# Performance work log

Hardware: AMD Instinct MI355X
Metric: run time of the kernel (lower is better)

## Reference

```python
import jax, jax.numpy as jnp
import numpy as np

EPS = 1e-8

def _l2norm(x):
    # normalize rows, guarding against zero norm like torch cosine similarity eps
    n = jnp.sqrt(jnp.sum(x * x, axis=-1, keepdims=True))
    return x / jnp.maximum(n, EPS)

def setup_inputs() -> dict:
    key = jax.random.key(0)
    k1, k2, k3 = jax.random.split(key, 3)
    Nq, Nk, D = 4096, 4096, 1024
    return {
        "queries": jax.random.normal(k1, (Nq, D), dtype=jnp.float32),
        "keys": jax.random.normal(k2, (Nk, D), dtype=jnp.float32),
        "values": jax.random.normal(k3, (Nk, D), dtype=jnp.float32),
    }

def reference(queries, keys, values):
    # CosineSimilarityMatrix(keys, queries): [Nk, Nq] pairwise cosine sims
    attn_weights = jnp.matmul(_l2norm(keys), _l2norm(queries).T)  # [Nk, Nq]
    # weighted sum over keys for each query
    weighted = jnp.matmul(attn_weights.T, values)  # [Nq, D]
    return (weighted, attn_weights)
```

## Files before the change

kernel.cpp:

```cpp
#include <hip/hip_runtime.h>


typedef unsigned short u16;
typedef unsigned int u32;
typedef unsigned char u8;
typedef float f32x4 __attribute__((ext_vector_type(4)));
typedef int int4v __attribute__((ext_vector_type(4)));
typedef __bf16 bf16x8 __attribute__((ext_vector_type(8)));

__device__ __forceinline__ u16 f2bf(float f) {
  u32 u = __builtin_bit_cast(u32, f);
  return (u16)((u + 0x7FFFu + ((u >> 16) & 1u)) >> 16);
}

__device__ __forceinline__ void gload16(const u16* g, u16* l) {
  __builtin_amdgcn_global_load_lds((__attribute__((address_space(1))) void*)(void*)g,
                                   (__attribute__((address_space(3))) void*)(void*)l, 16, 0, 0);
}
__device__ __forceinline__ void gload16b(const u8* g, u8* l) {
  __builtin_amdgcn_global_load_lds((__attribute__((address_space(1))) void*)(void*)g,
                                   (__attribute__((address_space(3))) void*)(void*)l, 16, 0, 0);
}

#define BARRIER() __builtin_amdgcn_s_barrier()
#define WAITVM(n) asm volatile("s_waitcnt vmcnt(" #n ")" ::: "memory")
#define WAITLGKM0() do { asm volatile("s_waitcnt lgkmcnt(0)" ::: "memory"); \
                         __builtin_amdgcn_sched_barrier(0); } while (0)

__global__ __launch_bounds__(256) void norm_transv_kernel(
    const float* __restrict__ q, const float* __restrict__ k,
    u16* __restrict__ qnb, u16* __restrict__ knb,
    u8* __restrict__ qnq, u8* __restrict__ knq,
    float* __restrict__ sclQ, float* __restrict__ sclK,
    const float* __restrict__ v, u16* __restrict__ vbT) {
  int bid = blockIdx.x, t = threadIdx.x;
  if (bid < 8192) {
    const bool isQ = (bid < 4096);
    const float* src = isQ ? q : k;
    u16* dst = isQ ? qnb : knb;
    u8* dst8 = isQ ? qnq : knq;
    float* scl = isQ ? sclQ : sclK;
    int row = bid & 4095;
    const float4 val = ((const float4*)(src + (size_t)row * 1024))[t];
    float s = val.x * val.x + val.y * val.y + val.z * val.z + val.w * val.w;
    float am = fmaxf(fmaxf(fabsf(val.x), fabsf(val.y)), fmaxf(fabsf(val.z), fabsf(val.w)));
    #pragma unroll
    for (int off = 32; off > 0; off >>= 1) {
      s += __shfl_xor(s, off, 64);
      am = fmaxf(am, __shfl_xor(am, off, 64));
    }
    __shared__ float2 red[4];
    if ((t & 63) == 0) red[t >> 6] = make_float2(s, am);
    __syncthreads();
    float tot = red[0].x + red[1].x + red[2].x + red[3].x;
    float amall = fmaxf(fmaxf(red[0].y, red[1].y), fmaxf(red[2].y, red[3].y));
    float inv = 1.0f / fmaxf(sqrtf(tot), 1e-8f);
    float rm = fmaxf(amall * inv, 1e-30f);
    float iq = 127.0f / rm;
    uint2 o;
    o.x = (u32)f2bf(val.x * inv) | ((u32)f2bf(val.y * inv) << 16);
    o.y = (u32)f2bf(val.z * inv) | ((u32)f2bf(val.w * inv) << 16);
    *(uint2*)(dst + (size_t)row * 1024 + t * 4) = o;
    int c0 = (int)rintf(val.x * inv * iq);
    int c1 = (int)rintf(val.y * inv * iq);
    int c2 = (int)rintf(val.z * inv * iq);
    int c3 = (int)rintf(val.w * inv * iq);
    u32 p = (u32)(c0 & 255) | ((u32)(c1 & 255) << 8) |
            ((u32)(c2 & 255) << 16) | ((u32)(c3 & 255) << 24);
    ((u32*)(dst8 + (size_t)row * 1024))[t] = p;
    if (t == 0) scl[row] = rm * (1.0f / 127.0f);
  } else {
    __shared__ __align__(16) float lds[64 * 64];
    int tix = bid - 8192;
    int r0 = (tix >> 4) * 64, c0 = (tix & 15) * 64;
    int ch = t & 15, lr = t >> 4;
    #pragma unroll
    for (int i = 0; i < 4; ++i) {
      int r = lr + i * 16;
      float4 val = *(const float4*)&v[(size_t)(r0 + r) * 1024 + c0 + ch * 4];
      int byteoff = r * 256 + ((ch * 16) ^ (((r >> 3) & 7) << 4));
      *(float4*)((char*)lds + byteoff) = val;
    }
    __syncthreads();
    int cch = t & 7, lrow = t >> 3;
    #pragma unroll
    for (int i = 0; i < 2; ++i) {
      int oc = lrow + i * 32;
      u16 vals[8];
      #pragma unroll
      for (int j = 0; j < 8; ++j) {
        int srl = cch * 8 + j;
        int byteoff = srl * 256 + (((oc >> 2) * 16) ^ (((srl >> 3) & 7) << 4)) + (oc & 3) * 4;
        vals[j] = f2bf(*(const float*)((const char*)lds + byteoff));
      }
      uint4 o;
      o.x = (u32)vals[0] | ((u32)vals[1] << 16);
      o.y = (u32)vals[2] | ((u32)vals[3] << 16);
      o.z = (u32)vals[4] | ((u32)vals[5] << 16);
      o.w = (u32)vals[6] | ((u32)vals[7] << 16);
      *(uint4*)&vbT[(size_t)(c0 + oc) * 4096 + r0 + cch * 8] = o;
    }
  }
}

__global__ __launch_bounds__(256) void transpose_bf16_kernel(
    const u16* __restrict__ src, u16* __restrict__ dst) {
  int b = blockIdx.x;
  int r0 = (b >> 4) * 64, c0 = (b & 15) * 64;
  __shared__ __align__(16) u16 lds[64 * 64];
  int t = threadIdx.x;
  int lrow = t >> 3, cch = t & 7;
  #pragma unroll
  for (int i = 0; i < 2; ++i) {
    int sr = lrow + i * 32;
    uint4 val = *(const uint4*)&src[(size_t)(r0 + sr) * 1024 + c0 + cch * 8];
    int byteoff = sr * 128 + ((cch * 16) ^ (((sr >> 3) & 7) << 4));
    *(uint4*)((char*)lds + byteoff) = val;
  }
  __syncthreads();
  #pragma unroll
  for (int i = 0; i < 2; ++i) {
    int oc = lrow + i * 32;
    u16 vals[8];
    #pragma unroll
    for (int j = 0; j < 8; ++j) {
      int srl = cch * 8 + j;
      int byteoff = srl * 128 + ((oc * 2) ^ (cch << 4));
      vals[j] = *(const u16*)((const char*)lds + byteoff);
    }
    uint4 o;
    o.x = (u32)vals[0] | ((u32)vals[1] << 16);
    o.y = (u32)vals[2] | ((u32)vals[3] << 16);
    o.z = (u32)vals[4] | ((u32)vals[5] << 16);
    o.w = (u32)vals[6] | ((u32)vals[7] << 16);
    *(uint4*)&dst[(size_t)(c0 + oc) * 4096 + r0 + cch * 8] = o;
  }
}

template<int BM, int BN, int MW, int NW>
__global__ __launch_bounds__(256) void gemm_abt(
    const u16* __restrict__ A, const u16* __restrict__ B, float* __restrict__ Cptr,
    int k_len, int lda, int ldb, int ldc, int plane) {
  static_assert(BM == 2 * MW * 16 && BN == 2 * NW * 16, "wave grid is 2x2");
  static_assert(BM / 32 + BN / 32 == 6, "WAITVM(6) literal assumes 6 loads/thread/stage");
  constexpr int TILE = (BM + BN) * 64;
  __shared__ __align__(16) u16 lds[3 * TILE];
  const int t = threadIdx.x, l = t & 63, w = t >> 6;
  const int tileM = blockIdx.y, tileN = blockIdx.x;
  const int k_start = blockIdx.z * k_len;
  Cptr += (size_t)blockIdx.z * plane;
  const int srow = l >> 3;
  const int cswz = ((l & 7) ^ srow) * 8;
  const u16* gA = A + (size_t)(tileM * BM) * lda + k_start + cswz;
  const u16* gB = B + (size_t)(tileN * BN) * ldb + k_start + cswz;
  const int slot0 = (l >> 4) ^ (l & 7);
  const int aoff0 = ((w >> 1) * MW * 16 + (l & 15)) * 64 + slot0 * 8;
  const int aoff1 = ((w >> 1) * MW * 16 + (l & 15)) * 64 + (slot0 ^ 4) * 8;
  const int boff0 = BM * 64 + ((w & 1) * NW * 16 + (l & 15)) * 64 + slot0 * 8;
  const int boff1 = BM * 64 + ((w & 1) * NW * 16 + (l & 15)) * 64 + (slot0 ^ 4) * 8;

  f32x4 acc[MW][NW];
  #pragma unroll
  for (int m = 0; m < MW; ++m)
    #pragma unroll
    for (int n = 0; n < NW; ++n) acc[m][n] = (f32x4){0.f, 0.f, 0.f, 0.f};

  auto stage = [&](int buf, int kof) {
    u16* bb = lds + buf * TILE;
    #pragma unroll
    for (int j = 0; j < BM / 32; ++j) {
      const int r = w * (BM / 4) + j * 8;
      gload16(gA + (size_t)(r + srow) * lda + kof, bb + r * 64);
    }
    #pragma unroll
    for (int j = 0; j < BN / 32; ++j) {
      const int r = w * (BN / 4) + j * 8;
      gload16(gB + (size_t)(r + srow) * ldb + kof, bb + BM * 64 + r * 64);
    }
  };

  bf16x8 av0[MW], bv0[NW], av1[MW], bv1[NW];
  const int nt = k_len >> 6;
  stage(0, 0);
  if (nt > 1) { stage(1, 64); WAITVM(6); }
  else        { WAITVM(0); }
  BARRIER();
  #pragma unroll
  for (int m = 0; m < MW; ++m) av0[m] = *(const bf16x8*)&lds[aoff0 + m * 1024];
  #pragma unroll
  for (int n = 0; n < NW; ++n) bv0[n] = *(const bf16x8*)&lds[boff0 + n * 1024];

  for (int i = 0; i < nt; ++i) {
    const u16* bb = lds + (i % 3) * TILE;
    if (i + 2 < nt) stage((i + 2) % 3, (i + 2) * 64);
    #pragma unroll
    for (int m = 0; m < MW; ++m) av1[m] = *(const bf16x8*)&bb[aoff1 + m * 1024];
    #pragma unroll
    for (int n = 0; n < NW; ++n) bv1[n] = *(const bf16x8*)&bb[boff1 + n * 1024];
    #pragma unroll
    for (int m = 0; m < MW; ++m)
      #pragma unroll
      for (int n = 0; n < NW; ++n)
        acc[m][n] = __builtin_amdgcn_mfma_f32_16x16x32_bf16(av0[m], bv0[n], acc[m][n], 0, 0, 0);
    #pragma unroll
    for (int m = 0; m < MW; ++m)
      #pragma unroll
      for (int n = 0; n < NW; ++n)
        acc[m][n] = __builtin_amdgcn_mfma_f32_16x16x32_bf16(av1[m], bv1[n], acc[m][n], 0, 0, 0);
    if (i + 1 < nt) {
      if (i + 2 < nt) { WAITVM(6); } else { WAITVM(0); }
    }
    BARRIER();
    if (i + 1 < nt) {
      const u16* nb = lds + ((i + 1) % 3) * TILE;
      #pragma unroll
      for (int m = 0; m < MW; ++m) av0[m] = *(const bf16x8*)&nb[aoff0 + m * 1024];
      #pragma unroll
      for (int n = 0; n < NW; ++n) bv0[n] = *(const bf16x8*)&nb[boff0 + n * 1024];
    }
  }

  const int orow = tileM * BM + (w >> 1) * MW * 16 + (l >> 4) * 4;
  const int ocol = tileN * BN + (w & 1) * NW * 16 + (l & 15);
  #pragma unroll
  for (int m = 0; m < MW; ++m)
    #pragma unroll
    for (int n = 0; n < NW; ++n)
      #pragma unroll
      for (int r = 0; r < 4; ++r)
        Cptr[(size_t)(orow + m * 16 + r) * ldc + (ocol + n * 16)] = acc[m][n][r];
}

__global__ __launch_bounds__(512, 2) void gemm256_i8(
    const u8* __restrict__ A8, const u8* __restrict__ B8, float* __restrict__ C,
    const float* __restrict__ P, u16* __restrict__ ctred,
    const float* __restrict__ sclK, const float* __restrict__ sclQ, int ntn) {
  __shared__ __align__(16) u8 lds8[131072];
  const int tid = threadIdx.x, l = tid & 63, w = tid >> 6;
  const int wm = w >> 2, wn = w & 3;
  const int nwg = gridDim.x * gridDim.y;
  const int bid = blockIdx.y * gridDim.x + blockIdx.x;
  const int swz = (bid & 7) * (nwg >> 3) + (bid >> 3);
  const int tileM = swz / ntn, tileN = swz % ntn;

  const int srow8 = l >> 3;
  const int cswzB = ((l & 7) ^ srow8) * 16;
  const u8* gA8 = A8 + (size_t)tileM * 256 * 1024 + cswzB;
  const u8* gB8 = B8 + (size_t)tileN * 256 * 1024 + cswzB;

#define STGJ(j, koff, bb) do { \
    gload16b(gA8 + (size_t)(w * 8 + 64 * (j) + srow8) * 1024 + (koff), \
             lds8 + (bb) + w * 1024 + (j) * 8192); \
    gload16b(gB8 + (size_t)(w * 8 + 64 * (j) + srow8) * 1024 + (koff), \
             lds8 + (bb) + 32768 + w * 1024 + (j) * 8192); } while (0)

  STGJ(0, 0, 0); STGJ(1, 0, 0); STGJ(2, 0, 0); STGJ(3, 0, 0);
  {
    const int base = bid * 4096 + tid * 8;
    f32x4 sa = *(const f32x4*)&P[base];
    f32x4 sb = *(const f32x4*)&P[base + 4];
    #pragma unroll
    for (int p = 1; p < 4; ++p) {
      sa += *(const f32x4*)&P[(size_t)p * 1048576 + base];
      sb += *(const f32x4*)&P[(size_t)p * 1048576 + base + 4];
    }
    uint4 o;
    o.x = (u32)f2bf(sa[0]) | ((u32)f2bf(sa[1]) << 16);
    o.y = (u32)f2bf(sa[2]) | ((u32)f2bf(sa[3]) << 16);
    o.z = (u32)f2bf(sb[0]) | ((u32)f2bf(sb[1]) << 16);
    o.w = (u32)f2bf(sb[2]) | ((u32)f2bf(sb[3]) << 16);
    *(uint4*)&ctred[base] = o;
  }
  WAITVM(0);
  BARRIER();

  const int fs = ((l >> 4) ^ (l & 7)) * 16;
  const int afrag0 = (wm * 128 + (l & 15)) * 128 + fs;
  const int bfrag0 = 32768 + (wn * 64 + (l & 15)) * 128 + fs;

  int4v acc[8][4];
  #pragma unroll
  for (int m = 0; m < 8; ++m)
    #pragma unroll
    for (int n = 0; n < 4; ++n) acc[m][n] = (int4v){0, 0, 0, 0};

#define MFMA16(AF, BF, MB) do { \
    __builtin_amdgcn_s_setprio(1); \
    _Pragma("unroll") \
    for (int m = 0; m < 4; ++m) { \
      _Pragma("unroll") \
      for (int n = 0; n < 4; ++n) \
        acc[(MB) + m][n] = __builtin_amdgcn_mfma_i32_16x16x64_i8(AF[m], BF[n], acc[(MB) + m][n], 0, 0, 0); \
    } \
    __builtin_amdgcn_s_setprio(0); } while (0)

  int4v A0[4], A1[4], B0[4], B1[4];
  #pragma unroll
  for (int m = 0; m < 4; ++m) A0[m] = *(const int4v*)&lds8[afrag0 + m * 2048];
  #pragma unroll
  for (int n = 0; n < 4; ++n) B0[n] = *(const int4v*)&lds8[bfrag0 + n * 2048];

  const int NT = 8;
  for (int t = 0; t < NT; ++t) {
    const int bb = (t & 1) << 16, nb = bb ^ 65536;
    const int nkoff = (t + 1) * 128;
    if (t + 1 < NT) STGJ(0, nkoff, nb);
    #pragma unroll
    for (int m = 0; m < 4; ++m) A1[m] = *(const int4v*)&lds8[bb + (afrag0 + (m + 4) * 2048)];
    WAITLGKM0();
    MFMA16(A0, B0, 0);
    if (t + 1 < NT) STGJ(1, nkoff, nb);
    #pragma unroll
    for (int m = 0; m < 4; ++m) A0[m] = *(const int4v*)&lds8[bb + ((afrag0 ^ 64) + m * 2048)];
    #pragma unroll
    for (int n = 0; n < 4; ++n) B1[n] = *(const int4v*)&lds8[bb + ((bfrag0 ^ 64) + n * 2048)];
    WAITLGKM0();
    MFMA16(A1, B0, 4);
    if (t + 1 < NT) STGJ(2, nkoff, nb);
    #pragma unroll
    for (int m = 0; m < 4; ++m) A1[m] = *(const int4v*)&lds8[bb + ((afrag0 ^ 64) + (m + 4) * 2048)];
    WAITLGKM0();
    MFMA16(A0, B1, 0);
    if (t + 1 < NT) STGJ(3, nkoff, nb);
    MFMA16(A1, B1, 4);
    if (t + 1 < NT) {
      WAITVM(0);
      BARRIER();
      #pragma unroll
      for (int m = 0; m < 4; ++m) A0[m] = *(const int4v*)&lds8[nb + (afrag0 + m * 2048)];
      #pragma unroll
      for (int n = 0; n < 4; ++n) B0[n] = *(const int4v*)&lds8[nb + (bfrag0 + n * 2048)];
    }
  }

  const int orow = tileM * 256 + wm * 128 + (l >> 4) * 4;
  const int ocol = tileN * 256 + wn * 64 + (l & 15);
  float sq[4];
  #pragma unroll
  for (int n = 0; n < 4; ++n) sq[n] = sclQ[ocol + n * 16];
  #pragma unroll
  for (int m = 0; m < 8; ++m) {
    const float4 sk4 = *(const float4*)&sclK[orow + m * 16];
    #pragma unroll
    for (int n = 0; n < 4; ++n)
      #pragma unroll
      for (int r = 0; r < 4; ++r)
        C[(size_t)(orow + m * 16 + r) * 4096 + (ocol + n * 16)] =
            (float)acc[m][n][r] * ((const float*)&sk4)[r] * sq[n];
  }
#undef STGJ
#undef MFMA16
}

extern "C" void kernel_launch(void* const* d_in, const int* in_sizes, int n_in,
                              void* d_out, int out_size, void* d_ws, size_t ws_size,
                              hipStream_t stream) {
  const float* q = (const float*)d_in[0];
  const float* k = (const float*)d_in[1];
  const float* v = (const float*)d_in[2];
  float* out = (float*)d_out;
  float* weighted = out;
  float* attn = out + 4194304;

  char* ws = (char*)d_ws;
  u16* qnb = (u16*)(ws);
  u16* knb = (u16*)(ws + (8u << 20));
  u16* knT = (u16*)(ws + (16u << 20));
  u16* vbT = (u16*)(ws + (24u << 20));
  u16* ct  = (u16*)(ws + (32u << 20));
  u8*  qnq = (u8*)(ws + (34u << 20));
  u8*  knq = (u8*)(ws + (38u << 20));
  float* sclQ = (float*)(ws + (42u << 20));
  float* sclK = (float*)(ws + (42u << 20) + 65536);

  norm_transv_kernel<<<9216, 256, 0, stream>>>(q, k, qnb, knb, qnq, knq, sclQ, sclK, v, vbT);
  transpose_bf16_kernel<<<1024, 256, 0, stream>>>(knb, knT);
  gemm_abt<128, 64, 4, 2><<<dim3(16, 8, 4), 256, 0, stream>>>(
      vbT, knT, weighted, 1024, 4096, 4096, 1024, 1048576);
  gemm256_i8<<<dim3(16, 16), 512, 0, stream>>>(
      knq, qnq, attn, weighted, ct, sclK, sclQ, 16);
  gemm_abt<128, 64, 4, 2><<<dim3(16, 32, 1), 256, 0, stream>>>(
      qnb, ct, weighted, 1024, 1024, 1024, 1024, 0);
}
```

Baseline: 82.50 us.

## Build transposed normalized K directly from fp32 keys and drop explicit LDS waits

New measurement: 83.07 us (median of 3 runs). No clear change (+0.7%).

```diff
diff --git a/kernel.cpp b/kernel.cpp
--- a/kernel.cpp
+++ b/kernel.cpp
@@ -24,20 +24,17 @@
 
 #define BARRIER() __builtin_amdgcn_s_barrier()
 #define WAITVM(n) asm volatile("s_waitcnt vmcnt(" #n ")" ::: "memory")
-#define WAITLGKM0() do { asm volatile("s_waitcnt lgkmcnt(0)" ::: "memory"); \
-                         __builtin_amdgcn_sched_barrier(0); } while (0)
 
 __global__ __launch_bounds__(256) void norm_transv_kernel(
     const float* __restrict__ q, const float* __restrict__ k,
-    u16* __restrict__ qnb, u16* __restrict__ knb,
+    u16* __restrict__ qnb,
     u8* __restrict__ qnq, u8* __restrict__ knq,
-    float* __restrict__ sclQ, float* __restrict__ sclK,
+    float* __restrict__ sclQ, float* __restrict__ sclK, float* __restrict__ invK,
     const float* __restrict__ v, u16* __restrict__ vbT) {
   int bid = blockIdx.x, t = threadIdx.x;
   if (bid < 8192) {
     const bool isQ = (bid < 4096);
     const float* src = isQ ? q : k;
-    u16* dst = isQ ? qnb : knb;
     u8* dst8 = isQ ? qnq : knq;
     float* scl = isQ ? sclQ : sclK;
     int row = bid & 4095;
@@ -57,10 +54,12 @@
     float inv = 1.0f / fmaxf(sqrtf(tot), 1e-8f);
     float rm = fmaxf(amall * inv, 1e-30f);
     float iq = 127.0f / rm;
-    uint2 o;
-    o.x = (u32)f2bf(val.x * inv) | ((u32)f2bf(val.y * inv) << 16);
-    o.y = (u32)f2bf(val.z * inv) | ((u32)f2bf(val.w * inv) << 16);
-    *(uint2*)(dst + (size_t)row * 1024 + t * 4) = o;
+    if (isQ) {
+      uint2 o;
+      o.x = (u32)f2bf(val.x * inv) | ((u32)f2bf(val.y * inv) << 16);
+      o.y = (u32)f2bf(val.z * inv) | ((u32)f2bf(val.w * inv) << 16);
+      *(uint2*)(qnb + (size_t)row * 1024 + t * 4) = o;
+    }
     int c0 = (int)rintf(val.x * inv * iq);
     int c1 = (int)rintf(val.y * inv * iq);
     int c2 = (int)rintf(val.z * inv * iq);
@@ -68,7 +67,10 @@
     u32 p = (u32)(c0 & 255) | ((u32)(c1 & 255) << 8) |
             ((u32)(c2 & 255) << 16) | ((u32)(c3 & 255) << 24);
     ((u32*)(dst8 + (size_t)row * 1024))[t] = p;
-    if (t == 0) scl[row] = rm * (1.0f / 127.0f);
+    if (t == 0) {
+      scl[row] = rm * (1.0f / 127.0f);
+      if (!isQ) invK[row] = inv;
+    }
   } else {
     __shared__ __align__(16) float lds[64 * 64];
     int tix = bid - 8192;
@@ -103,21 +105,26 @@
   }
 }
 
-__global__ __launch_bounds__(256) void transpose_bf16_kernel(
-    const u16* __restrict__ src, u16* __restrict__ dst) {
+__global__ __launch_bounds__(256) void transpose_k_kernel(
+    const float* __restrict__ k, const float* __restrict__ invK,
+    u16* __restrict__ knT) {
   int b = blockIdx.x;
   int r0 = (b >> 4) * 64, c0 = (b & 15) * 64;
-  __shared__ __align__(16) u16 lds[64 * 64];
+  __shared__ __align__(16) float lds[64 * 64];
   int t = threadIdx.x;
-  int lrow = t >> 3, cch = t & 7;
-  #pragma unroll
-  for (int i = 0; i < 2; ++i) {
-    int sr = lrow + i * 32;
-    uint4 val = *(const uint4*)&src[(size_t)(r0 + sr) * 1024 + c0 + cch * 8];
-    int byteoff = sr * 128 + ((cch * 16) ^ (((sr >> 3) & 7) << 4));
-    *(uint4*)((char*)lds + byteoff) = val;
+  int ch = t & 15, lr = t >> 4;
+  #pragma unroll
+  for (int i = 0; i < 4; ++i) {
+    int r = lr + i * 16;
+    float4 val = *(const float4*)&k[(size_t)(r0 + r) * 1024 + c0 + ch * 4];
+    int byteoff = r * 256 + ((ch * 16) ^ (((r >> 3) & 7) << 4));
+    *(float4*)((char*)lds + byteoff) = val;
   }
   __syncthreads();
+  int cch = t & 7, lrow = t >> 3;
+  float invv[8];
+  *(float4*)&invv[0] = *(const float4*)&invK[r0 + cch * 8];
+  *(float4*)&invv[4] = *(const float4*)&invK[r0 + cch * 8 + 4];
   #pragma unroll
   for (int i = 0; i < 2; ++i) {
     int oc = lrow + i * 32;
@@ -125,15 +132,15 @@
     #pragma unroll
     for (int j = 0; j < 8; ++j) {
       int srl = cch * 8 + j;
-      int byteoff = srl * 128 + ((oc * 2) ^ (cch << 4));
-      vals[j] = *(const u16*)((const char*)lds + byteoff);
+      int byteoff = srl * 256 + (((oc >> 2) * 16) ^ (((srl >> 3) & 7) << 4)) + (oc & 3) * 4;
+      vals[j] = f2bf(*(const float*)((const char*)lds + byteoff) * invv[j]);
     }
     uint4 o;
     o.x = (u32)vals[0] | ((u32)vals[1] << 16);
     o.y = (u32)vals[2] | ((u32)vals[3] << 16);
     o.z = (u32)vals[4] | ((u32)vals[5] << 16);
     o.w = (u32)vals[6] | ((u32)vals[7] << 16);
-    *(uint4*)&dst[(size_t)(c0 + oc) * 4096 + r0 + cch * 8] = o;
+    *(uint4*)&knT[(size_t)(c0 + oc) * 4096 + r0 + cch * 8] = o;
   }
 }
 
@@ -307,19 +314,16 @@
     if (t + 1 < NT) STGJ(0, nkoff, nb);
     #pragma unroll
     for (int m = 0; m < 4; ++m) A1[m] = *(const int4v*)&lds8[bb + (afrag0 + (m + 4) * 2048)];
-    WAITLGKM0();
     MFMA16(A0, B0, 0);
     if (t + 1 < NT) STGJ(1, nkoff, nb);
     #pragma unroll
     for (int m = 0; m < 4; ++m) A0[m] = *(const int4v*)&lds8[bb + ((afrag0 ^ 64) + m * 2048)];
     #pragma unroll
     for (int n = 0; n < 4; ++n) B1[n] = *(const int4v*)&lds8[bb + ((bfrag0 ^ 64) + n * 2048)];
-    WAITLGKM0();
     MFMA16(A1, B0, 4);
     if (t + 1 < NT) STGJ(2, nkoff, nb);
     #pragma unroll
     for (int m = 0; m < 4; ++m) A1[m] = *(const int4v*)&lds8[bb + ((afrag0 ^ 64) + (m + 4) * 2048)];
-    WAITLGKM0();
     MFMA16(A0, B1, 0);
     if (t + 1 < NT) STGJ(3, nkoff, nb);
     MFMA16(A1, B1, 4);
@@ -364,17 +368,17 @@
 
   char* ws = (char*)d_ws;
   u16* qnb = (u16*)(ws);
-  u16* knb = (u16*)(ws + (8u << 20));
-  u16* knT = (u16*)(ws + (16u << 20));
-  u16* vbT = (u16*)(ws + (24u << 20));
-  u16* ct  = (u16*)(ws + (32u << 20));
-  u8*  qnq = (u8*)(ws + (34u << 20));
-  u8*  knq = (u8*)(ws + (38u << 20));
-  float* sclQ = (float*)(ws + (42u << 20));
-  float* sclK = (float*)(ws + (42u << 20) + 65536);
-
-  norm_transv_kernel<<<9216, 256, 0, stream>>>(q, k, qnb, knb, qnq, knq, sclQ, sclK, v, vbT);
-  transpose_bf16_kernel<<<1024, 256, 0, stream>>>(knb, knT);
+  u16* knT = (u16*)(ws + (8u << 20));
+  u16* vbT = (u16*)(ws + (16u << 20));
+  u16* ct  = (u16*)(ws + (24u << 20));
+  u8*  qnq = (u8*)(ws + (26u << 20));
+  u8*  knq = (u8*)(ws + (30u << 20));
+  float* sclQ = (float*)(ws + (34u << 20));
+  float* sclK = (float*)(ws + (34u << 20) + 65536);
+  float* invK = (float*)(ws + (34u << 20) + 131072);
+
+  norm_transv_kernel<<<9216, 256, 0, stream>>>(q, k, qnb, qnq, knq, sclQ, sclK, invK, v, vbT);
+  transpose_k_kernel<<<1024, 256, 0, stream>>>(k, invK, knT);
   gemm_abt<128, 64, 4, 2><<<dim3(16, 8, 4), 256, 0, stream>>>(
       vbT, knT, weighted, 1024, 4096, 4096, 1024, 1048576);
   gemm256_i8<<<dim3(16, 16), 512, 0, stream>>>(
```
